# Optimization experiments

Measured on AMD Instinct MI355X. Metric: run time of the kernel, lower is better.

Reference implementation:

```python
import jax, jax.numpy as jnp
import numpy as np


def setup_inputs() -> dict:
    key = jax.random.key(0)
    k1, k2, k3, k4, k5 = jax.random.split(key, 5)
    N, M = 8192, 8192
    ref_kpts = jax.random.normal(k1, (N, 3), dtype=jnp.float32)
    src_kpts = jax.random.normal(k2, (M, 3), dtype=jnp.float32)
    gt_transform = jax.random.normal(k3, (4, 4), dtype=jnp.float32)
    ref_sigma = jax.random.uniform(k4, (N,), dtype=jnp.float32)
    src_sigma = jax.random.uniform(k5, (M,), dtype=jnp.float32)
    return {"ref_kpts": ref_kpts, "src_kpts": src_kpts, "gt_transform": gt_transform,
            "ref_sigma": ref_sigma, "src_sigma": src_sigma}


def reference(ref_kpts, src_kpts, gt_transform, ref_sigma, src_sigma):
    # apply_transform: rigid SE(3): p @ R^T + t
    R = gt_transform[:3, :3]
    t = gt_transform[:3, 3]
    kpts2 = src_kpts @ R.T + t  # [M, 3]
    # pairwise euclidean distances [N, M]
    diff = jnp.linalg.norm(ref_kpts[:, None, :] - kpts2[None, :, :], axis=-1)
    # forward direction: for each ref point, nearest transformed src point
    min_dist_fwd = jnp.min(diff, axis=-1)        # [N]
    idx_fwd = jnp.argmin(diff, axis=-1)          # [N]
    sigma_fwd = (ref_sigma + src_sigma[idx_fwd]) * 0.5
    forward_loss = jnp.mean(jnp.log(sigma_fwd) + min_dist_fwd / sigma_fwd)
    # backward direction: for each src point, nearest ref point
    min_dist_bwd = jnp.min(diff, axis=0)         # [M]
    idx_bwd = jnp.argmin(diff, axis=0)           # [M]
    sigma_bwd = (src_sigma + ref_sigma[idx_bwd]) * 0.5
    backward_loss = jnp.mean(jnp.log(sigma_bwd) + min_dist_bwd / sigma_bwd)
    return forward_loss + backward_loss
```

## Files before the change

kernel.cpp:

```cpp
#include <hip/hip_runtime.h>
#include <math.h>

typedef float v2f __attribute__((ext_vector_type(2)));

#define TPB 256
#define IPT 4
#define JS  64

__global__ __launch_bounds__(256) void setup_kernel(
    const float* __restrict__ ref, const float* __restrict__ src,
    const float* __restrict__ T,
    float* __restrict__ rx, float* __restrict__ ry, float* __restrict__ rz,
    float* __restrict__ rw,
    float* __restrict__ sx, float* __restrict__ sy, float* __restrict__ sz,
    float* __restrict__ sw,
    unsigned long long* __restrict__ packF,
    unsigned long long* __restrict__ packB,
    float* __restrict__ out, int N, int M) {
  int i = blockIdx.x * blockDim.x + threadIdx.x;
  if (i < M) {
    float x = src[3 * i], y = src[3 * i + 1], z = src[3 * i + 2];
    float tx = T[0] * x + T[1] * y + T[2]  * z + T[3];
    float ty = T[4] * x + T[5] * y + T[6]  * z + T[7];
    float tz = T[8] * x + T[9] * y + T[10] * z + T[11];
    sx[i] = tx; sy[i] = ty; sz[i] = tz;
    sw[i] = tx * tx + ty * ty + tz * tz;
    packB[i] = ~0ull;
  }
  if (i < N) {
    float x = ref[3 * i], y = ref[3 * i + 1], z = ref[3 * i + 2];
    rx[i] = x; ry[i] = y; rz[i] = z;
    rw[i] = x * x + y * y + z * z;
    packF[i] = ~0ull;
  }
  if (i == 0) {
    out[0] = 0.0f;
    rx[N] = 0.f; ry[N] = 0.f; rz[N] = 0.f; rw[N] = INFINITY;
    sx[M] = 0.f; sy[M] = 0.f; sz[M] = 0.f; sw[M] = INFINITY;
  }
}

__device__ __forceinline__ unsigned int sortable(float f) {
  unsigned int u = __float_as_uint(f);
  return u ^ ((unsigned int)((int)u >> 31) | 0x80000000u);
}

__global__ __launch_bounds__(TPB) void pairs_kernel(
    const float* __restrict__ rx, const float* __restrict__ ry,
    const float* __restrict__ rz, const float* __restrict__ rw,
    const float* __restrict__ sx, const float* __restrict__ sy,
    const float* __restrict__ sz, const float* __restrict__ sw,
    unsigned long long* __restrict__ packF,
    unsigned long long* __restrict__ packB,
    int N, int M, int nbF) {
  int b = blockIdx.x;
  const float *px_, *py_, *pz_, *ox, *oy, *oz, *ow;
  unsigned long long* pack;
  int selfN, otherN;
  if (b < nbF) {
    px_ = rx; py_ = ry; pz_ = rz;
    ox = sx; oy = sy; oz = sz; ow = sw;
    pack = packF; selfN = N; otherN = M;
  } else {
    b -= nbF;
    px_ = sx; py_ = sy; pz_ = sz;
    ox = rx; oy = ry; oz = rz; ow = rw;
    pack = packB; selfN = M; otherN = N;
  }
  const int ib = b / JS, jb = b % JS;
  const int i0 = ib * (TPB * IPT) + threadIdx.x;

  float ax[IPT], ay[IPT], az[IPT], mind[IPT];
  int mini[IPT];
#pragma unroll
  for (int k = 0; k < IPT; k++) {
    int i = i0 + k * TPB;
    int ic = (i < selfN) ? i : (selfN - 1);
    ax[k] = -2.0f * px_[ic]; ay[k] = -2.0f * py_[ic]; az[k] = -2.0f * pz_[ic];
    mind[k] = INFINITY; mini[k] = 0;
  }

  int chunk = (otherN + JS - 1) / JS;
  chunk = (chunk + 1) & ~1;
  const int j0 = jb * chunk;
  const int jcount = min(chunk, otherN - j0);

#pragma unroll 4
  for (int jj = 0; jj < jcount; jj += 2) {
    v2f qx = *(const v2f*)(ox + j0 + jj);
    v2f qy = *(const v2f*)(oy + j0 + jj);
    v2f qz = *(const v2f*)(oz + j0 + jj);
    v2f qw = *(const v2f*)(ow + j0 + jj);
#pragma unroll
    for (int k = 0; k < IPT; k++) {
      v2f t = __builtin_elementwise_fma((v2f){ax[k], ax[k]}, qx, qw);
      t = __builtin_elementwise_fma((v2f){ay[k], ay[k]}, qy, t);
      t = __builtin_elementwise_fma((v2f){az[k], az[k]}, qz, t);
      if (t.x < mind[k]) { mind[k] = t.x; mini[k] = jj; }
      if (t.y < mind[k]) { mind[k] = t.y; mini[k] = jj + 1; }
    }
  }

#pragma unroll
  for (int k = 0; k < IPT; k++) {
    int i = i0 + k * TPB;
    if (i < selfN && jcount > 0) {
      unsigned long long p = ((unsigned long long)sortable(mind[k]) << 32) |
                             (unsigned int)(j0 + mini[k]);
      atomicMin(&pack[i], p);
    }
  }
}

__global__ __launch_bounds__(256) void finalize_kernel(
    const unsigned long long* __restrict__ packF,
    const unsigned long long* __restrict__ packB,
    const float* __restrict__ rx, const float* __restrict__ ry,
    const float* __restrict__ rz,
    const float* __restrict__ sx, const float* __restrict__ sy,
    const float* __restrict__ sz,
    const float* __restrict__ ref_sigma, const float* __restrict__ src_sigma,
    float* __restrict__ out, int N, int M) {
  int gid = blockIdx.x * blockDim.x + threadIdx.x;
  float term = 0.f;
  if (gid < N) {
    int idx = (int)(packF[gid] & 0xffffffffu);
    float dx = rx[gid] - sx[idx], dy = ry[gid] - sy[idx],
          dz = rz[gid] - sz[idx];
    float d = sqrtf(dx * dx + dy * dy + dz * dz);
    float sigma = 0.5f * (ref_sigma[gid] + src_sigma[idx]);
    term = (logf(sigma) + d / sigma) * (1.0f / (float)N);
  } else if (gid < N + M) {
    int j = gid - N;
    int idx = (int)(packB[j] & 0xffffffffu);
    float dx = sx[j] - rx[idx], dy = sy[j] - ry[idx], dz = sz[j] - rz[idx];
    float d = sqrtf(dx * dx + dy * dy + dz * dz);
    float sigma = 0.5f * (src_sigma[j] + ref_sigma[idx]);
    term = (logf(sigma) + d / sigma) * (1.0f / (float)M);
  }
#pragma unroll
  for (int o = 32; o > 0; o >>= 1) term += __shfl_down(term, o, 64);
  __shared__ float wsum[4];
  const int lane = threadIdx.x & 63, wid = threadIdx.x >> 6;
  if (lane == 0) wsum[wid] = term;
  __syncthreads();
  if (threadIdx.x == 0)
    atomicAdd(out, wsum[0] + wsum[1] + wsum[2] + wsum[3]);
}

extern "C" void kernel_launch(void* const* d_in, const int* in_sizes, int n_in,
                              void* d_out, int out_size, void* d_ws,
                              size_t ws_size, hipStream_t stream) {
  const float* ref_kpts  = (const float*)d_in[0];
  const float* src_kpts  = (const float*)d_in[1];
  const float* gt        = (const float*)d_in[2];
  const float* ref_sigma = (const float*)d_in[3];
  const float* src_sigma = (const float*)d_in[4];
  float* out = (float*)d_out;

  const int N = in_sizes[0] / 3;
  const int M = in_sizes[1] / 3;

  const int NP = (N + 1 + 3) & ~3;
  const int MP = (M + 1 + 3) & ~3;
  float* f = (float*)d_ws;
  float* rx = f;            float* ry = f + NP;
  float* rz = f + 2 * NP;   float* rw = f + 3 * NP;
  float* sx = f + 4 * NP;           float* sy = f + 4 * NP + MP;
  float* sz = f + 4 * NP + 2 * MP;  float* sw = f + 4 * NP + 3 * MP;
  unsigned long long* packF = (unsigned long long*)(f + 4 * NP + 4 * MP);
  unsigned long long* packB = packF + N;

  int nPts = (N > M) ? N : M;
  setup_kernel<<<(nPts + 255) / 256, 256, 0, stream>>>(
      ref_kpts, src_kpts, gt, rx, ry, rz, rw, sx, sy, sz, sw, packF, packB,
      out, N, M);

  const int ibF = (N + TPB * IPT - 1) / (TPB * IPT);
  const int ibB = (M + TPB * IPT - 1) / (TPB * IPT);
  const int nbF = ibF * JS;
  const int nbB = ibB * JS;
  pairs_kernel<<<nbF + nbB, TPB, 0, stream>>>(rx, ry, rz, rw, sx, sy, sz, sw,
                                              packF, packB, N, M, nbF);

  finalize_kernel<<<(N + M + 255) / 256, 256, 0, stream>>>(
      packF, packB, rx, ry, rz, sx, sy, sz, ref_sigma, src_sigma, out, N, M);
}
```

Measured before the change: 86.69 us.

## Interleave point coordinates in pairs layout and double j-split count

Point coordinates and squared norms are now stored as interleaved groups of two points (x0 x1 y0 y1 z0 z1 w0 w1), so the inner loop fetches one pair of points with two 16-byte loads instead of four 8-byte loads from separate arrays. The j-dimension split grows from 64 to 128 chunks, doubling the block count and halving per-block work. The pairs kernel also gets a launch-bounds occupancy hint. More blocks means more atomicMin traffic on the pack arrays in exchange for better load balance.

Result: no change. 87.98 us (+1.5%).

```diff
diff --git a/kernel.cpp b/kernel.cpp
--- a/kernel.cpp
+++ b/kernel.cpp
@@ -2,18 +2,17 @@
 #include <math.h>
 
 typedef float v2f __attribute__((ext_vector_type(2)));
+typedef float v4f __attribute__((ext_vector_type(4)));
 
 #define TPB 256
 #define IPT 4
-#define JS  64
+#define JS  128
+
 
 __global__ __launch_bounds__(256) void setup_kernel(
     const float* __restrict__ ref, const float* __restrict__ src,
     const float* __restrict__ T,
-    float* __restrict__ rx, float* __restrict__ ry, float* __restrict__ rz,
-    float* __restrict__ rw,
-    float* __restrict__ sx, float* __restrict__ sy, float* __restrict__ sz,
-    float* __restrict__ sw,
+    float* __restrict__ refI, float* __restrict__ srcI,
     unsigned long long* __restrict__ packF,
     unsigned long long* __restrict__ packB,
     float* __restrict__ out, int N, int M) {
@@ -23,20 +22,33 @@
     float tx = T[0] * x + T[1] * y + T[2]  * z + T[3];
     float ty = T[4] * x + T[5] * y + T[6]  * z + T[7];
     float tz = T[8] * x + T[9] * y + T[10] * z + T[11];
-    sx[i] = tx; sy[i] = ty; sz[i] = tz;
-    sw[i] = tx * tx + ty * ty + tz * tz;
+    int base = 8 * (i >> 1) + (i & 1);
+    srcI[base]     = tx;
+    srcI[base + 2] = ty;
+    srcI[base + 4] = tz;
+    srcI[base + 6] = tx * tx + ty * ty + tz * tz;
     packB[i] = ~0ull;
   }
   if (i < N) {
     float x = ref[3 * i], y = ref[3 * i + 1], z = ref[3 * i + 2];
-    rx[i] = x; ry[i] = y; rz[i] = z;
-    rw[i] = x * x + y * y + z * z;
+    int base = 8 * (i >> 1) + (i & 1);
+    refI[base]     = x;
+    refI[base + 2] = y;
+    refI[base + 4] = z;
+    refI[base + 6] = x * x + y * y + z * z;
     packF[i] = ~0ull;
   }
   if (i == 0) {
     out[0] = 0.0f;
-    rx[N] = 0.f; ry[N] = 0.f; rz[N] = 0.f; rw[N] = INFINITY;
-    sx[M] = 0.f; sy[M] = 0.f; sz[M] = 0.f; sw[M] = INFINITY;
+#pragma unroll
+    for (int e = 0; e < 2; e++) {
+      int bn = 8 * ((N + e) >> 1) + ((N + e) & 1);
+      refI[bn] = 0.f; refI[bn + 2] = 0.f; refI[bn + 4] = 0.f;
+      refI[bn + 6] = INFINITY;
+      int bm = 8 * ((M + e) >> 1) + ((M + e) & 1);
+      srcI[bm] = 0.f; srcI[bm + 2] = 0.f; srcI[bm + 4] = 0.f;
+      srcI[bm + 6] = INFINITY;
+    }
   }
 }
 
@@ -45,27 +57,20 @@
   return u ^ ((unsigned int)((int)u >> 31) | 0x80000000u);
 }
 
-__global__ __launch_bounds__(TPB) void pairs_kernel(
-    const float* __restrict__ rx, const float* __restrict__ ry,
-    const float* __restrict__ rz, const float* __restrict__ rw,
-    const float* __restrict__ sx, const float* __restrict__ sy,
-    const float* __restrict__ sz, const float* __restrict__ sw,
+__global__ __launch_bounds__(TPB, 4) void pairs_kernel(
+    const float* __restrict__ refI, const float* __restrict__ srcI,
     unsigned long long* __restrict__ packF,
     unsigned long long* __restrict__ packB,
     int N, int M, int nbF) {
   int b = blockIdx.x;
-  const float *px_, *py_, *pz_, *ox, *oy, *oz, *ow;
+  const float *selfI, *otherI;
   unsigned long long* pack;
   int selfN, otherN;
   if (b < nbF) {
-    px_ = rx; py_ = ry; pz_ = rz;
-    ox = sx; oy = sy; oz = sz; ow = sw;
-    pack = packF; selfN = N; otherN = M;
+    selfI = refI; otherI = srcI; pack = packF; selfN = N; otherN = M;
   } else {
     b -= nbF;
-    px_ = sx; py_ = sy; pz_ = sz;
-    ox = rx; oy = ry; oz = rz; ow = rw;
-    pack = packB; selfN = M; otherN = N;
+    selfI = srcI; otherI = refI; pack = packB; selfN = M; otherN = N;
   }
   const int ib = b / JS, jb = b % JS;
   const int i0 = ib * (TPB * IPT) + threadIdx.x;
@@ -76,7 +81,10 @@
   for (int k = 0; k < IPT; k++) {
     int i = i0 + k * TPB;
     int ic = (i < selfN) ? i : (selfN - 1);
-    ax[k] = -2.0f * px_[ic]; ay[k] = -2.0f * py_[ic]; az[k] = -2.0f * pz_[ic];
+    int base = 8 * (ic >> 1) + (ic & 1);
+    ax[k] = -2.0f * selfI[base];
+    ay[k] = -2.0f * selfI[base + 2];
+    az[k] = -2.0f * selfI[base + 4];
     mind[k] = INFINITY; mini[k] = 0;
   }
 
@@ -85,12 +93,16 @@
   const int j0 = jb * chunk;
   const int jcount = min(chunk, otherN - j0);
 
+  const v4f* og = (const v4f*)(otherI + 4 * j0);
+
 #pragma unroll 4
   for (int jj = 0; jj < jcount; jj += 2) {
-    v2f qx = *(const v2f*)(ox + j0 + jj);
-    v2f qy = *(const v2f*)(oy + j0 + jj);
-    v2f qz = *(const v2f*)(oz + j0 + jj);
-    v2f qw = *(const v2f*)(ow + j0 + jj);
+    v4f A = og[jj];
+    v4f B = og[jj + 1];
+    v2f qx = __builtin_shufflevector(A, A, 0, 1);
+    v2f qy = __builtin_shufflevector(A, A, 2, 3);
+    v2f qz = __builtin_shufflevector(B, B, 0, 1);
+    v2f qw = __builtin_shufflevector(B, B, 2, 3);
 #pragma unroll
     for (int k = 0; k < IPT; k++) {
       v2f t = __builtin_elementwise_fma((v2f){ax[k], ax[k]}, qx, qw);
@@ -115,25 +127,29 @@
 __global__ __launch_bounds__(256) void finalize_kernel(
     const unsigned long long* __restrict__ packF,
     const unsigned long long* __restrict__ packB,
-    const float* __restrict__ rx, const float* __restrict__ ry,
-    const float* __restrict__ rz,
-    const float* __restrict__ sx, const float* __restrict__ sy,
-    const float* __restrict__ sz,
+    const float* __restrict__ refI, const float* __restrict__ srcI,
     const float* __restrict__ ref_sigma, const float* __restrict__ src_sigma,
     float* __restrict__ out, int N, int M) {
   int gid = blockIdx.x * blockDim.x + threadIdx.x;
   float term = 0.f;
   if (gid < N) {
     int idx = (int)(packF[gid] & 0xffffffffu);
-    float dx = rx[gid] - sx[idx], dy = ry[gid] - sy[idx],
-          dz = rz[gid] - sz[idx];
+    int sb = 8 * (gid >> 1) + (gid & 1);
+    int ob = 8 * (idx >> 1) + (idx & 1);
+    float dx = refI[sb]     - srcI[ob];
+    float dy = refI[sb + 2] - srcI[ob + 2];
+    float dz = refI[sb + 4] - srcI[ob + 4];
     float d = sqrtf(dx * dx + dy * dy + dz * dz);
     float sigma = 0.5f * (ref_sigma[gid] + src_sigma[idx]);
     term = (logf(sigma) + d / sigma) * (1.0f / (float)N);
   } else if (gid < N + M) {
     int j = gid - N;
     int idx = (int)(packB[j] & 0xffffffffu);
-    float dx = sx[j] - rx[idx], dy = sy[j] - ry[idx], dz = sz[j] - rz[idx];
+    int sb = 8 * (j >> 1) + (j & 1);
+    int ob = 8 * (idx >> 1) + (idx & 1);
+    float dx = srcI[sb]     - refI[ob];
+    float dy = srcI[sb + 2] - refI[ob + 2];
+    float dz = srcI[sb + 4] - refI[ob + 4];
     float d = sqrtf(dx * dx + dy * dy + dz * dz);
     float sigma = 0.5f * (src_sigma[j] + ref_sigma[idx]);
     term = (logf(sigma) + d / sigma) * (1.0f / (float)M);
@@ -161,28 +177,25 @@
   const int N = in_sizes[0] / 3;
   const int M = in_sizes[1] / 3;
 
-  const int NP = (N + 1 + 3) & ~3;
-  const int MP = (M + 1 + 3) & ~3;
+  const int NG8 = 8 * ((N + 3) / 2);
+  const int MG8 = 8 * ((M + 3) / 2);
   float* f = (float*)d_ws;
-  float* rx = f;            float* ry = f + NP;
-  float* rz = f + 2 * NP;   float* rw = f + 3 * NP;
-  float* sx = f + 4 * NP;           float* sy = f + 4 * NP + MP;
-  float* sz = f + 4 * NP + 2 * MP;  float* sw = f + 4 * NP + 3 * MP;
-  unsigned long long* packF = (unsigned long long*)(f + 4 * NP + 4 * MP);
+  float* refI = f;
+  float* srcI = f + NG8;
+  unsigned long long* packF = (unsigned long long*)(f + NG8 + MG8);
   unsigned long long* packB = packF + N;
 
   int nPts = (N > M) ? N : M;
   setup_kernel<<<(nPts + 255) / 256, 256, 0, stream>>>(
-      ref_kpts, src_kpts, gt, rx, ry, rz, rw, sx, sy, sz, sw, packF, packB,
-      out, N, M);
+      ref_kpts, src_kpts, gt, refI, srcI, packF, packB, out, N, M);
 
   const int ibF = (N + TPB * IPT - 1) / (TPB * IPT);
   const int ibB = (M + TPB * IPT - 1) / (TPB * IPT);
   const int nbF = ibF * JS;
   const int nbB = ibB * JS;
-  pairs_kernel<<<nbF + nbB, TPB, 0, stream>>>(rx, ry, rz, rw, sx, sy, sz, sw,
-                                              packF, packB, N, M, nbF);
+  pairs_kernel<<<nbF + nbB, TPB, 0, stream>>>(refI, srcI, packF, packB,
+                                              N, M, nbF);
 
   finalize_kernel<<<(N + M + 255) / 256, 256, 0, stream>>>(
-      packF, packB, rx, ry, rz, sx, sy, sz, ref_sigma, src_sigma, out, N, M);
-}
+      packF, packB, refI, srcI, ref_sigma, src_sigma, out, N, M);
+}
```
